# Performance work log

Hardware: AMD Instinct MI355X
Metric: run time of the kernel (lower is better)

## Reference

```python
import jax, jax.numpy as jnp
import numpy as np

B, S, D_IN, D_OUT = 4, 2048, 1024, 1024

def setup_inputs() -> dict:
    key = jax.random.key(0)
    k0, k1, k2, k3 = jax.random.split(key, 4)
    sc = 1.0 / np.sqrt(D_IN)
    return {
        "x": jax.random.normal(k0, (B, S, D_IN), dtype=jnp.float32),
        "wq": jax.random.normal(k1, (D_OUT, D_IN), dtype=jnp.float32) * sc,
        "wk": jax.random.normal(k2, (D_OUT, D_IN), dtype=jnp.float32) * sc,
        "wv": jax.random.normal(k3, (D_OUT, D_IN), dtype=jnp.float32) * sc,
    }

def reference(x, wq, wk, wv):
    # Linear (no bias): y = x @ W.T, W shaped [d_out, d_in]
    q = jnp.einsum("bsd,ed->bse", x, wq)
    k = jnp.einsum("bsd,ed->bse", x, wk)
    v = jnp.einsum("bsd,ed->bse", x, wv)
    scores = jnp.einsum("bqe,bke->bqk", q, k)  # [B,S,S]
    n = x.shape[1]
    causal = jnp.triu(jnp.ones((n, n), dtype=bool), k=1)  # True above diagonal -> masked
    scores = jnp.where(causal, -jnp.inf, scores)
    attn = jax.nn.softmax(scores / jnp.sqrt(jnp.asarray(k.shape[-1], scores.dtype)), axis=-1)
    # dropout p=0.0 -> identity
    return jnp.einsum("bqk,bke->bqe", attn, v)
```

## Files before the change

### kernel.cpp

```cpp
#include <hip/hip_runtime.h>

#define Bb 4
#define Ss 2048
#define Dd 1024

typedef unsigned short u16;
typedef __bf16 bf16x8 __attribute__((ext_vector_type(8)));
typedef float  f32x4  __attribute__((ext_vector_type(4)));

__device__ inline u16 f2bf(float f) {
  union { float f; unsigned u; } x; x.f = f;
  unsigned u = x.u;
  return (u16)((u + 0x7fffu + ((u >> 16) & 1u)) >> 16);
}
__device__ inline float bf2f(u16 h) {
  union { unsigned u; float f; } x; x.u = ((unsigned)h) << 16;
  return x.f;
}

__device__ static inline void gl_lds16(const u16* g, u16* l) {
  __builtin_amdgcn_global_load_lds((__attribute__((address_space(1))) const void*)g,
                                   (__attribute__((address_space(3))) void*)l,
                                   16, 0, 0);
}

__device__ static inline void qbar() {
  asm volatile("" ::: "memory");
  __builtin_amdgcn_s_barrier();
  asm volatile("" ::: "memory");
}

template <int GATEN>
__device__ __forceinline__ void qk_gate() {
  if constexpr (GATEN == 8) asm volatile("s_waitcnt vmcnt(8)" ::: "memory");
  else if constexpr (GATEN == 4) asm volatile("s_waitcnt vmcnt(4)" ::: "memory");
  else if constexpr (GATEN == 0) asm volatile("s_waitcnt vmcnt(0)" ::: "memory");
}

__global__ __launch_bounds__(256) void cast_all(const float* __restrict__ x,
                                                const float* __restrict__ wq,
                                                const float* __restrict__ wk,
                                                const float* __restrict__ wv,
                                                u16* __restrict__ xb,
                                                u16* __restrict__ wb,
                                                float* __restrict__ lsum) {
  int id = blockIdx.x;
  if (id < 8) {
    float4 z = {0.f, 0.f, 0.f, 0.f};
    ((float4*)lsum)[id * 256 + threadIdx.x] = z;
  }
  const float* src; u16* dst; int off;
  if (id < 2048) {
    src = x; dst = xb; off = id * 4096;
  } else {
    int wi = id - 2048;
    int w = wi >> 8;
    src = (w == 0) ? wq : (w == 1) ? wk : wv;
    dst = wb + (size_t)w * Dd * Dd;
    off = (wi & 255) * 4096;
  }
#pragma unroll
  for (int t = 0; t < 4; t++) {
    int i = off + t * 1024 + threadIdx.x * 4;
    float4 v = *(const float4*)(src + i);
    unsigned p0 = (unsigned)f2bf(v.x) | ((unsigned)f2bf(v.y) << 16);
    unsigned p1 = (unsigned)f2bf(v.z) | ((unsigned)f2bf(v.w) << 16);
    uint2 p; p.x = p0; p.y = p1;
    *(uint2*)(dst + i) = p;
  }
}

#define BM 128
#define BN 128

__device__ inline void gemm_tile(const u16* __restrict__ A, int lda,
                                 const u16* __restrict__ Bp, int ldb,
                                 int kBeg, int kEnd,
                                 u16* lds, f32x4 acc[4][4]) {
  u16* lA0 = lds;
  u16* lB0 = lds + 4096;
  u16* lA1 = lds + 8192;
  u16* lB1 = lds + 12288;
  const int tid  = threadIdx.x;
  const int lane = tid & 63, wave = tid >> 6;
  const int quad = lane >> 4, r16 = lane & 15;
  const int wm = (wave & 1) * 64, wn = (wave >> 1) * 64;
  const int r0 = tid >> 2, part = tid & 3;

  for (int k0 = kBeg; k0 < kEnd; k0 += 64) {
    __syncthreads();
#pragma unroll
    for (int q = 0; q < 2; q++) {
      int row = q * 64 + r0;
      int s8 = (q * 256 + tid) * 8;
      const u16* ga = A  + (size_t)row * lda + k0 + part * 8;
      const u16* gb = Bp + (size_t)row * ldb + k0 + part * 8;
      gl_lds16(ga,      lA0 + s8);
      gl_lds16(gb,      lB0 + s8);
      gl_lds16(ga + 32, lA1 + s8);
      gl_lds16(gb + 32, lB1 + s8);
    }
    __syncthreads();
#pragma unroll
    for (int h = 0; h < 2; h++) {
      const u16* la = h ? lA1 : lA0;
      const u16* lb = h ? lB1 : lB0;
      bf16x8 fa[4], fb[4];
#pragma unroll
      for (int t = 0; t < 4; t++)
        fa[t] = *(const bf16x8*)(la + (wm + t * 16 + r16) * 32 + quad * 8);
#pragma unroll
      for (int t = 0; t < 4; t++)
        fb[t] = *(const bf16x8*)(lb + (wn + t * 16 + r16) * 32 + quad * 8);
#pragma unroll
      for (int tm = 0; tm < 4; tm++)
#pragma unroll
        for (int tn = 0; tn < 4; tn++)
          acc[tm][tn] = __builtin_amdgcn_mfma_f32_16x16x32_bf16(fa[tm], fb[tn],
                                                                acc[tm][tn], 0, 0, 0);
    }
  }
}

#define QBK 32

__global__ __launch_bounds__(512, 2) void qkv_gemm256(const u16* __restrict__ xb,
                                                      const u16* __restrict__ wb,
                                                      u16* __restrict__ qkv) {
  __shared__ __align__(16) u16 sh[4 * 16384];
  u16* const shf = sh;

  const int id  = blockIdx.x;
  const int swz = (id & 7) * 48 + (id >> 3);
  const int zi  = swz >> 7;
  const int rem = swz & 127;
  const int mt  = rem >> 2, nt = rem & 3;
  const int row0 = mt * 256, col0 = nt * 256;
  const u16* A  = xb + (size_t)row0 * Dd;
  const u16* Bp = wb + (size_t)zi * Dd * Dd + (size_t)col0 * Dd;

  const int tid  = threadIdx.x;
  const int lane = tid & 63, wave = tid >> 6;
  const int wr = wave >> 2, wc = wave & 3;
  const int quad = lane >> 4, r16 = lane & 15;

  const int pA0 = tid, pA1 = tid + 512;
  const int r0a = pA0 >> 2, c0a = pA0 & 3;
  const int r1a = pA1 >> 2, c1a = pA1 & 3;
  const u16* aS0 = A  + (size_t)r0a * Dd + (size_t)((c0a ^ ((r0a >> 1) & 3)) * 8);
  const u16* aS1 = A  + (size_t)r1a * Dd + (size_t)((c1a ^ ((r1a >> 1) & 3)) * 8);
  const u16* bS0 = Bp + (size_t)r0a * Dd + (size_t)((c0a ^ ((r0a >> 1) & 3)) * 8);
  const u16* bS1 = Bp + (size_t)r1a * Dd + (size_t)((c1a ^ ((r1a >> 1) & 3)) * 8);

  auto stgA = [&](int S) {
    u16* d = shf + (S & 3) * 16384;
    gl_lds16(aS0 + (size_t)S * QBK, d + pA0 * 8);
    gl_lds16(aS1 + (size_t)S * QBK, d + pA1 * 8);
  };
  auto stgB = [&](int S) {
    u16* d = shf + (S & 3) * 16384 + 8192;
    gl_lds16(bS0 + (size_t)S * QBK, d + pA0 * 8);
    gl_lds16(bS1 + (size_t)S * QBK, d + pA1 * 8);
  };

  const int chq  = (quad ^ ((r16 >> 1) & 3)) * 8;
  const int idxA = (wr * 128 + r16) * 32 + chq;
  const int idxB = (wc * 64  + r16) * 32 + chq;

  f32x4 acc[8][4];
#pragma unroll
  for (int m = 0; m < 8; m++)
#pragma unroll
    for (int n = 0; n < 4; n++) acc[m][n] = (f32x4){0.f, 0.f, 0.f, 0.f};
  bf16x8 fb[4];

#define QKV_TILE(U, STG_S, GATEN)                                              \
  {                                                                            \
    const u16* lA = shf + (U) * 16384;                                         \
    const u16* lB = lA + 8192;                                                 \
    bf16x8 fa[4];                                                              \
    _Pragma("unroll") for (int m = 0; m < 4; m++)                              \
        fa[m] = *(const bf16x8*)(lA + idxA + m * 512);                         \
    _Pragma("unroll") for (int n = 0; n < 4; n++)                              \
        fb[n] = *(const bf16x8*)(lB + idxB + n * 512);                         \
    if ((STG_S) >= 0) stgA(STG_S);                                             \
    qbar();                                                                    \
    __builtin_amdgcn_s_setprio(1);                                             \
    _Pragma("unroll") for (int m = 0; m < 4; m++)                              \
      _Pragma("unroll") for (int n = 0; n < 4; n++)                            \
        acc[m][n] = __builtin_amdgcn_mfma_f32_16x16x32_bf16(fa[m], fb[n],      \
                                                            acc[m][n], 0, 0, 0); \
    __builtin_amdgcn_s_setprio(0);                                             \
    qbar();                                                                    \
    _Pragma("unroll") for (int m = 0; m < 4; m++)                              \
        fa[m] = *(const bf16x8*)(lA + idxA + (m + 4) * 512);                   \
    if ((STG_S) >= 0) stgB(STG_S);                                             \
    qk_gate<GATEN>();                                                          \
    qbar();                                                                    \
    __builtin_amdgcn_s_setprio(1);                                             \
    _Pragma("unroll") for (int m = 0; m < 4; m++)                              \
      _Pragma("unroll") for (int n = 0; n < 4; n++)                            \
        acc[m + 4][n] = __builtin_amdgcn_mfma_f32_16x16x32_bf16(fa[m], fb[n],  \
                                                                acc[m + 4][n], 0, 0, 0); \
    __builtin_amdgcn_s_setprio(0);                                             \
    qbar();                                                                    \
  }

  stgA(0); stgB(0); stgA(1); stgB(1); stgA(2); stgB(2);
  asm volatile("s_waitcnt vmcnt(8)" ::: "memory");
  qbar();

#pragma unroll 1
  for (int T = 0; T < 28; T++) QKV_TILE(T & 3, T + 3, 8);
  QKV_TILE(0, 31, 8);
  QKV_TILE(1, -1, 4);
  QKV_TILE(2, -1, 0);
  QKV_TILE(3, -1, -1);
#undef QKV_TILE

  u16* out = qkv + (size_t)zi * ((size_t)Bb * Ss * Dd);
#pragma unroll
  for (int m = 0; m < 8; m++) {
    int rr = row0 + wr * 128 + m * 16 + quad * 4;
#pragma unroll
    for (int n = 0; n < 4; n++) {
      int cc = col0 + wc * 64 + n * 16 + r16;
#pragma unroll
      for (int r = 0; r < 4; r++)
        out[(size_t)(rr + r) * Dd + cc] = f2bf(acc[m][n][r]);
    }
  }
}

__global__ __launch_bounds__(256) void scores_fused(const u16* __restrict__ qb,
                                                    const u16* __restrict__ kb,
                                                    const u16* __restrict__ vb,
                                                    u16* __restrict__ sc,
                                                    u16* __restrict__ vt,
                                                    float* __restrict__ lsum) {
  __shared__ __align__(16) u16 shmem[16384];
  const int id = blockIdx.x;
  const int tid = threadIdx.x;

  if (id >= 544) {
    const int bid = id - 544;
    u16 (*t)[72] = (u16(*)[72])shmem;
    for (int u = bid; u < 2048; u += 480) {
      const int b = u >> 9, rem = u & 511;
      const int e0 = (rem >> 5) * 64, s0 = (rem & 31) * 64;
      const u16* src = vb + (size_t)b * Ss * Dd;
      u16* dst = vt + (size_t)b * Dd * Ss;
      if (u != bid) __syncthreads();
#pragma unroll
      for (int gg = tid; gg < 512; gg += 256) {
        int row = gg >> 3, prt = gg & 7;
        uint4 v = *(const uint4*)(src + (size_t)(s0 + row) * Dd + e0 + prt * 8);
        const u16* pv = (const u16*)&v;
#pragma unroll
        for (int jj = 0; jj < 8; jj++) t[prt * 8 + jj][row] = pv[jj];
      }
      __syncthreads();
#pragma unroll
      for (int gg = tid; gg < 512; gg += 256) {
        int ee = gg >> 3, prt = gg & 7;
        uint4 v = *(const uint4*)(&t[ee][prt * 8]);
        *(uint4*)(dst + (size_t)(e0 + ee) * Ss + s0 + prt * 8) = v;
      }
    }
    return;
  }

  const int xcd = id & 7, j = id >> 3;
  const int b = j / 17, tloc = j - b * 17;
  const int t = xcd * 17 + tloc;
  int it = (int)((sqrtf(8.f * (float)t + 1.f) - 1.f) * 0.5f);
  while ((it + 1) * (it + 2) / 2 <= t) it++;
  while (it * (it + 1) / 2 > t) it--;
  const int jt = t - it * (it + 1) / 2;

  const u16* A  = qb + (size_t)b * Ss * Dd + (size_t)it * BM * Dd;
  const u16* Bp = kb + (size_t)b * Ss * Dd + (size_t)jt * BN * Dd;
  f32x4 acc[4][4];
  const f32x4 zero = {0.f, 0.f, 0.f, 0.f};
#pragma unroll
  for (int tm = 0; tm < 4; tm++)
#pragma unroll
    for (int tn = 0; tn < 4; tn++) acc[tm][tn] = zero;

  gemm_tile(A, Dd, Bp, Dd, 0, Dd, shmem, acc);

  u16* out = sc + (size_t)b * Ss * Ss;
  float* lr = lsum + (size_t)b * Ss;
  const int lane = tid & 63, wave = tid >> 6;
  const int quad = lane >> 4, r16 = lane & 15;
  const int wm = (wave & 1) * 64, wn = (wave >> 1) * 64;
#pragma unroll
  for (int tm = 0; tm < 4; tm++) {
    float psum[4] = {0.f, 0.f, 0.f, 0.f};
#pragma unroll
    for (int tn = 0; tn < 4; tn++) {
      int rr = it * BM + wm + tm * 16 + quad * 4;
      int cc = jt * BN + wn + tn * 16 + r16;
#pragma unroll
      for (int r = 0; r < 4; r++) {
        float p = 0.f;
        u16 h = 0;
        if (cc <= rr + r) {
          h = f2bf(__expf(acc[tm][tn][r] * 0.03125f));
          p = bf2f(h);
        }
        out[(size_t)(rr + r) * Ss + cc] = h;
        psum[r] += p;
      }
    }
#pragma unroll
    for (int r = 0; r < 4; r++) {
      float s = psum[r];
      s += __shfl_xor(s, 1);
      s += __shfl_xor(s, 2);
      s += __shfl_xor(s, 4);
      s += __shfl_xor(s, 8);
      if (r16 == 0) {
        int row = it * BM + wm + tm * 16 + quad * 4 + r;
        atomicAdd(&lr[row], s);
      }
    }
  }
}

__global__ __launch_bounds__(256) void pv_gemm(const u16* __restrict__ sc,
                                               const u16* __restrict__ vt,
                                               const float* __restrict__ lsum,
                                               float* __restrict__ out) {
  __shared__ __align__(16) u16 shmem[16384];
  const int idx = blockIdx.x;
  const int xcd = idx & 7, slot = idx >> 3;
  const int qp = slot >> 3, col = slot & 7;
  const int b = qp & 3;
  const int it = (qp >> 2) ? (15 - xcd) : xcd;
  const int row0 = it * BM;
  const int col0 = col * BN;
  const u16* A  = sc + (size_t)b * Ss * Ss + (size_t)row0 * Ss;
  const u16* Bp = vt + (size_t)b * Dd * Ss + (size_t)col0 * Ss;
  f32x4 acc[4][4];
  const f32x4 zero = {0.f, 0.f, 0.f, 0.f};
#pragma unroll
  for (int tm = 0; tm < 4; tm++)
#pragma unroll
    for (int tn = 0; tn < 4; tn++) acc[tm][tn] = zero;

  gemm_tile(A, Ss, Bp, Ss, 0, row0 + BM, shmem, acc);

  float* o = out + (size_t)b * Ss * Dd;
  const float* lr = lsum + (size_t)b * Ss;
  const int lane = threadIdx.x & 63, wave = threadIdx.x >> 6;
  const int quad = lane >> 4, r16 = lane & 15;
  const int wm = (wave & 1) * 64, wn = (wave >> 1) * 64;
#pragma unroll
  for (int tm = 0; tm < 4; tm++) {
    int rbase = row0 + wm + tm * 16 + quad * 4;
    float s0 = 1.f / lr[rbase], s1 = 1.f / lr[rbase + 1];
    float s2 = 1.f / lr[rbase + 2], s3 = 1.f / lr[rbase + 3];
#pragma unroll
    for (int tn = 0; tn < 4; tn++) {
      int cc = col0 + wn + tn * 16 + r16;
      o[(size_t)(rbase + 0) * Dd + cc] = acc[tm][tn][0] * s0;
      o[(size_t)(rbase + 1) * Dd + cc] = acc[tm][tn][1] * s1;
      o[(size_t)(rbase + 2) * Dd + cc] = acc[tm][tn][2] * s2;
      o[(size_t)(rbase + 3) * Dd + cc] = acc[tm][tn][3] * s3;
    }
  }
}

extern "C" void kernel_launch(void* const* d_in, const int* in_sizes, int n_in,
                              void* d_out, int out_size, void* d_ws, size_t ws_size,
                              hipStream_t stream) {
  const float* x  = (const float*)d_in[0];
  const float* wq = (const float*)d_in[1];
  const float* wk = (const float*)d_in[2];
  const float* wv = (const float*)d_in[3];
  float* out = (float*)d_out;
  char* ws = (char*)d_ws;
  if (ws_size < 106987520u) return;

  u16* qkv  = (u16*)(ws);
  u16* sc   = (u16*)(ws + 50331648u);
  u16* xb   = (u16*)(ws + 83886080u);
  u16* vt   = xb;
  u16* wb   = (u16*)(ws + 100663296u);
  float* lsum = (float*)(ws + 106954752u);

  const size_t nQ = (size_t)Bb * Ss * Dd;

  cast_all<<<2816, 256, 0, stream>>>(x, wq, wk, wv, xb, wb, lsum);
  qkv_gemm256<<<384, 512, 0, stream>>>(xb, wb, qkv);
  scores_fused<<<1024, 256, 0, stream>>>(qkv, qkv + nQ, qkv + 2 * nQ, sc, vt, lsum);
  pv_gemm<<<512, 256, 0, stream>>>(sc, vt, lsum, out);
}
```

Baseline: 242.6 us.

## Shrink QKV GEMM tile to 256x128 and simplify pipeline to single-phase

Replaces the 256x256-tile QKV projection GEMM with a 256x128 tile over 768 blocks. Each of the 8 waves now owns a 64x64 output region, so the two half-step MFMA phases per K-step collapse into one, with a single combined staging of A and B. Waitcnt thresholds and the LDS buffer size are adjusted to match three loads per stage. The aim is better load balance across CUs (768 blocks instead of 384) and fewer barriers per K-step. The cost is lower arithmetic intensity, with more global and LDS traffic per FLOP, and launch bounds relaxed to 1 block per CU.

```diff
diff --git a/kernel.cpp b/kernel.cpp
--- a/kernel.cpp
+++ b/kernel.cpp
@@ -32,8 +32,8 @@
 
 template <int GATEN>
 __device__ __forceinline__ void qk_gate() {
-  if constexpr (GATEN == 8) asm volatile("s_waitcnt vmcnt(8)" ::: "memory");
-  else if constexpr (GATEN == 4) asm volatile("s_waitcnt vmcnt(4)" ::: "memory");
+  if constexpr (GATEN == 6) asm volatile("s_waitcnt vmcnt(6)" ::: "memory");
+  else if constexpr (GATEN == 3) asm volatile("s_waitcnt vmcnt(3)" ::: "memory");
   else if constexpr (GATEN == 0) asm volatile("s_waitcnt vmcnt(0)" ::: "memory");
 }
 
@@ -124,24 +124,23 @@
 
 #define QBK 32
 
-__global__ __launch_bounds__(512, 2) void qkv_gemm256(const u16* __restrict__ xb,
-                                                      const u16* __restrict__ wb,
-                                                      u16* __restrict__ qkv) {
-  __shared__ __align__(16) u16 sh[4 * 16384];
-  u16* const shf = sh;
+__global__ __launch_bounds__(512, 1) void qkv_gemm3(const u16* __restrict__ xb,
+                                                    const u16* __restrict__ wb,
+                                                    u16* __restrict__ qkv) {
+  __shared__ __align__(16) u16 sh[4 * 12288];
 
   const int id  = blockIdx.x;
-  const int swz = (id & 7) * 48 + (id >> 3);
-  const int zi  = swz >> 7;
-  const int rem = swz & 127;
-  const int mt  = rem >> 2, nt = rem & 3;
-  const int row0 = mt * 256, col0 = nt * 256;
+  const int swz = (id & 7) * 96 + (id >> 3);
+  const int zi  = swz >> 8;
+  const int rem = swz & 255;
+  const int mt  = rem >> 3, nt = rem & 7;
+  const int row0 = mt * 256, col0 = nt * 128;
   const u16* A  = xb + (size_t)row0 * Dd;
   const u16* Bp = wb + (size_t)zi * Dd * Dd + (size_t)col0 * Dd;
 
   const int tid  = threadIdx.x;
   const int lane = tid & 63, wave = tid >> 6;
-  const int wr = wave >> 2, wc = wave & 3;
+  const int wr = wave >> 1, wc = wave & 1;
   const int quad = lane >> 4, r16 = lane & 15;
 
   const int pA0 = tid, pA1 = tid + 512;
@@ -150,40 +149,35 @@
   const u16* aS0 = A  + (size_t)r0a * Dd + (size_t)((c0a ^ ((r0a >> 1) & 3)) * 8);
   const u16* aS1 = A  + (size_t)r1a * Dd + (size_t)((c1a ^ ((r1a >> 1) & 3)) * 8);
   const u16* bS0 = Bp + (size_t)r0a * Dd + (size_t)((c0a ^ ((r0a >> 1) & 3)) * 8);
-  const u16* bS1 = Bp + (size_t)r1a * Dd + (size_t)((c1a ^ ((r1a >> 1) & 3)) * 8);
-
-  auto stgA = [&](int S) {
-    u16* d = shf + (S & 3) * 16384;
+
+  auto stg = [&](int S) {
+    u16* d = sh + (S & 3) * 12288;
     gl_lds16(aS0 + (size_t)S * QBK, d + pA0 * 8);
     gl_lds16(aS1 + (size_t)S * QBK, d + pA1 * 8);
+    gl_lds16(bS0 + (size_t)S * QBK, d + 8192 + pA0 * 8);
   };
-  auto stgB = [&](int S) {
-    u16* d = shf + (S & 3) * 16384 + 8192;
-    gl_lds16(bS0 + (size_t)S * QBK, d + pA0 * 8);
-    gl_lds16(bS1 + (size_t)S * QBK, d + pA1 * 8);
-  };
 
   const int chq  = (quad ^ ((r16 >> 1) & 3)) * 8;
-  const int idxA = (wr * 128 + r16) * 32 + chq;
-  const int idxB = (wc * 64  + r16) * 32 + chq;
-
-  f32x4 acc[8][4];
-#pragma unroll
-  for (int m = 0; m < 8; m++)
+  const int idxA = (wr * 64 + r16) * 32 + chq;
+  const int idxB = (wc * 64 + r16) * 32 + chq;
+
+  f32x4 acc[4][4];
+#pragma unroll
+  for (int m = 0; m < 4; m++)
 #pragma unroll
     for (int n = 0; n < 4; n++) acc[m][n] = (f32x4){0.f, 0.f, 0.f, 0.f};
-  bf16x8 fb[4];
-
-#define QKV_TILE(U, STG_S, GATEN)                                              \
+
+#define QTILE(U, STG_S, GATEN)                                                 \
   {                                                                            \
-    const u16* lA = shf + (U) * 16384;                                         \
+    const u16* lA = sh + (U) * 12288;                                          \
     const u16* lB = lA + 8192;                                                 \
-    bf16x8 fa[4];                                                              \
+    bf16x8 fa[4], fb[4];                                                       \
     _Pragma("unroll") for (int m = 0; m < 4; m++)                              \
         fa[m] = *(const bf16x8*)(lA + idxA + m * 512);                         \
     _Pragma("unroll") for (int n = 0; n < 4; n++)                              \
         fb[n] = *(const bf16x8*)(lB + idxB + n * 512);                         \
-    if ((STG_S) >= 0) stgA(STG_S);                                             \
+    if ((STG_S) >= 0) stg(STG_S);                                              \
+    qk_gate<GATEN>();                                                          \
     qbar();                                                                    \
     __builtin_amdgcn_s_setprio(1);                                             \
     _Pragma("unroll") for (int m = 0; m < 4; m++)                              \
@@ -192,36 +186,23 @@
                                                             acc[m][n], 0, 0, 0); \
     __builtin_amdgcn_s_setprio(0);                                             \
     qbar();                                                                    \
-    _Pragma("unroll") for (int m = 0; m < 4; m++)                              \
-        fa[m] = *(const bf16x8*)(lA + idxA + (m + 4) * 512);                   \
-    if ((STG_S) >= 0) stgB(STG_S);                                             \
-    qk_gate<GATEN>();                                                          \
-    qbar();                                                                    \
-    __builtin_amdgcn_s_setprio(1);                                             \
-    _Pragma("unroll") for (int m = 0; m < 4; m++)                              \
-      _Pragma("unroll") for (int n = 0; n < 4; n++)                            \
-        acc[m + 4][n] = __builtin_amdgcn_mfma_f32_16x16x32_bf16(fa[m], fb[n],  \
-                                                                acc[m + 4][n], 0, 0, 0); \
-    __builtin_amdgcn_s_setprio(0);                                             \
-    qbar();                                                                    \
-  }
-
-  stgA(0); stgB(0); stgA(1); stgB(1); stgA(2); stgB(2);
-  asm volatile("s_waitcnt vmcnt(8)" ::: "memory");
+  }
+
+  stg(0); stg(1); stg(2);
+  asm volatile("s_waitcnt vmcnt(6)" ::: "memory");
   qbar();
 
 #pragma unroll 1
-  for (int T = 0; T < 28; T++) QKV_TILE(T & 3, T + 3, 8);
-  QKV_TILE(0, 31, 8);
-  QKV_TILE(1, -1, 4);
-  QKV_TILE(2, -1, 0);
-  QKV_TILE(3, -1, -1);
-#undef QKV_TILE
+  for (int T = 0; T < 29; T++) QTILE(T & 3, T + 3, 6);
+  QTILE(1, -1, 3);
+  QTILE(2, -1, 0);
+  QTILE(3, -1, -1);
+#undef QTILE
 
   u16* out = qkv + (size_t)zi * ((size_t)Bb * Ss * Dd);
 #pragma unroll
-  for (int m = 0; m < 8; m++) {
-    int rr = row0 + wr * 128 + m * 16 + quad * 4;
+  for (int m = 0; m < 4; m++) {
+    int rr = row0 + wr * 64 + m * 16 + quad * 4;
 #pragma unroll
     for (int n = 0; n < 4; n++) {
       int cc = col0 + wc * 64 + n * 16 + r16;
@@ -393,7 +374,7 @@
   const size_t nQ = (size_t)Bb * Ss * Dd;
 
   cast_all<<<2816, 256, 0, stream>>>(x, wq, wk, wv, xb, wb, lsum);
-  qkv_gemm256<<<384, 512, 0, stream>>>(xb, wb, qkv);
+  qkv_gemm3<<<768, 512, 0, stream>>>(xb, wb, qkv);
   scores_fused<<<1024, 256, 0, stream>>>(qkv, qkv + nQ, qkv + 2 * nQ, sc, vt, lsum);
   pv_gemm<<<512, 256, 0, stream>>>(sc, vt, lsum, out);
 }
```

After: 238.7 us. No clear change (-1.6%).
